# Kernel tuning notes

Hardware: AMD Instinct MI355X
Metric: run time of the kernel (lower is better)

Reference implementation:

```python
import jax, jax.numpy as jnp
import numpy as np

EPS = 1e-8

def leaky(x):
    return jnp.where(x >= 0, x, 0.1 * x)

def gln(y, gamma, beta, axes):
    # global layer norm: normalize over all non-batch axes given
    mean = jnp.mean(y, axis=axes, keepdims=True)
    var = jnp.mean((y - mean) ** 2, axis=axes, keepdims=True)
    return gamma * (y - mean) / jnp.sqrt(var + EPS) + beta

def conv1d(x, w, b, stride, padding):
    # x: [N, Cin, T], w: [Cout, Cin, K]
    out = jax.lax.conv_general_dilated(
        x, w, window_strides=(stride,), padding=[(padding, padding)],
        dimension_numbers=('NCH', 'OIH', 'NCH'))
    return out + b[None, :, None]

def setup_inputs() -> dict:
    key = jax.random.key(0)
    ks = jax.random.split(key, 8)
    M, C, B, T = 4, 2, 128, 2000
    feature = jax.random.normal(ks[0], (M, B, T), jnp.float32)
    mask = jax.random.uniform(ks[1], (M, C, B, T), jnp.float32)
    # Conv2d(B*C -> 1, 1x1) weight stored as [C, B] (xavier-ish scale)
    w2d = jax.random.normal(ks[2], (C, B), jnp.float32) * (1.0 / np.sqrt(C * B))
    b2d = jnp.zeros((), jnp.float32)
    g2d = jnp.ones((), jnp.float32)    # GLN_2D(1) gamma
    be2d = jnp.zeros((), jnp.float32)  # GLN_2D(1) beta
    # Conv1d stack: 128->256 (k3,s2,p1), 256->256 (k3,s2,p1), 256->1 (k1,s1)
    w1 = jax.random.normal(ks[3], (256, B, 3), jnp.float32) * (1.0 / np.sqrt(B * 3))
    b1 = jnp.zeros((256,), jnp.float32)
    g1 = jnp.ones((1, 256, 1), jnp.float32)
    bb1 = jnp.zeros((1, 256, 1), jnp.float32)
    w2 = jax.random.normal(ks[4], (256, 256, 3), jnp.float32) * (1.0 / np.sqrt(256 * 3))
    b2 = jnp.zeros((256,), jnp.float32)
    g2 = jnp.ones((1, 256, 1), jnp.float32)
    bb2 = jnp.zeros((1, 256, 1), jnp.float32)
    w3 = jax.random.normal(ks[5], (1, 256, 1), jnp.float32) * (1.0 / np.sqrt(256))
    b3 = jnp.zeros((1,), jnp.float32)
    return dict(feature=feature, mask=mask, w2d=w2d, b2d=b2d, g2d=g2d, be2d=be2d,
                w1=w1, b1=b1, g1=g1, bb1=bb1, w2=w2, b2=b2, g2=g2, bb2=bb2,
                w3=w3, b3=b3)

def reference(feature, mask, w2d, b2d, g2d, be2d,
              w1, b1, g1, bb1, w2, b2, g2, bb2, w3, b3):
    # torch: d_in = einsum('bft,bcpt->bcfpt').view(B, C*F, P, T) -> Conv2d(C*F->1, 1x1)
    # With F == P == B, the viewed channel index is (c*F + f), so the 1x1 conv is
    #   d[b,p,t] = sum_{c,f} w2d[c,f] * feature[b,f,t] * mask[b,c,p,t] + b2d
    # expressed as a fused two-step contraction (same math, no 5D materialization):
    a = jnp.einsum('cf,bft->bct', w2d, feature)        # [M, C, T]
    d = jnp.einsum('bct,bcpt->bpt', a, mask) + b2d     # [M, P, T]
    d = d[:, None]                                     # [M, 1, P, T]
    d = gln(d, g2d, be2d, axes=(1, 2, 3))              # GLN_2D(1)
    d = leaky(d)
    x = d[:, 0]                                        # squeeze(1) -> [M, B, T]
    x = leaky(gln(conv1d(x, w1, b1, 2, 1), g1, bb1, (1, 2)))
    x = leaky(gln(conv1d(x, w2, b2, 2, 1), g2, bb2, (1, 2)))
    x = conv1d(x, w3, b3, 1, 0)                        # [M, 1, 500]
    return x
```

## Files before the change

kernel.cpp:

```cpp
#include <hip/hip_runtime.h>
#include <hip/hip_bf16.h>

#define EPS 1e-8f
typedef unsigned short ushortT;
typedef __bf16 bf16x8 __attribute__((ext_vector_type(8)));
typedef float f32x4 __attribute__((ext_vector_type(4)));
union B8 { uint4 u; bf16x8 v; };

__device__ __forceinline__ float leaky(float x) { return x >= 0.f ? x : 0.1f * x; }

__device__ __forceinline__ ushortT f2bf(float v) {
    unsigned u = __float_as_uint(v);
    return (ushortT)((u + 0x7fffu + ((u >> 16) & 1u)) >> 16);
}

__device__ __forceinline__ void block_reduce2(float& s, float& q, float* red) {
    __syncthreads();
    #pragma unroll
    for (int off = 32; off > 0; off >>= 1) {
        s += __shfl_down(s, off, 64);
        q += __shfl_down(q, off, 64);
    }
    const int wid = threadIdx.x >> 6, lane = threadIdx.x & 63;
    if (lane == 0) { red[wid] = s; red[4 + wid] = q; }
    __syncthreads();
    if (threadIdx.x == 0) {
        s = red[0] + red[1] + red[2] + red[3];
        q = red[4] + red[5] + red[6] + red[7];
    }
}

__device__ __forceinline__ void stats_from_partials(const float* __restrict__ partials,
                                                    int n, float nrm,
                                                    float* red, float* stat) {
    float s = 0.f, q = 0.f;
    if ((int)threadIdx.x < n) {
        s = partials[threadIdx.x * 2];
        q = partials[threadIdx.x * 2 + 1];
    }
    block_reduce2(s, q, red);
    if (threadIdx.x == 0) {
        float mean = s * nrm;
        float var  = fmaxf(q * nrm - mean * mean, 0.f);
        stat[0] = mean;
        stat[1] = rsqrtf(var + EPS);
    }
    __syncthreads();
}

__global__ void ka(const float* __restrict__ feature, const float* __restrict__ mask,
                   const float* __restrict__ w2d, const float* __restrict__ b2d,
                   const float* __restrict__ w1, const float* __restrict__ w2,
                   ushortT* __restrict__ w1b, ushortT* __restrict__ w2b,
                   float* __restrict__ dT, float* __restrict__ p0out) {
    if (blockIdx.x >= 63) {
        int p = (blockIdx.x - 63) * 4 + blockIdx.y;
        int base = (p < 96 ? p : p - 96) * 1024 + threadIdx.x * 4;
        const float* src = (p < 96) ? (w1 + base) : (w2 + base);
        ushortT* dst = (p < 96) ? (w1b + base) : (w2b + base);
        float4 v = *(const float4*)src;
        ushort4 o;
        o.x = f2bf(v.x); o.y = f2bf(v.y); o.z = f2bf(v.z); o.w = f2bf(v.w);
        *(ushort4*)dst = o;
        return;
    }
    __shared__ float4 apart[2][32][8];
    __shared__ float4 a0s4[8], a1s4[8];
    __shared__ float Xt[32][132];
    __shared__ float red[8];
    const int b = blockIdx.y;
    const int t0 = blockIdx.x * 32;
    const int tq = threadIdx.x & 7;
    const int hi = threadIdx.x >> 3;

    {
        const int tbase = t0 + tq * 4;
        float4 s0 = {0.f, 0.f, 0.f, 0.f}, s1 = s0;
        if (tbase + 3 < 2000) {
            const float* fb = feature + ((size_t)b * 128 + hi * 4) * 2000 + tbase;
            float4 wa = *(const float4*)(w2d + hi * 4);
            float4 wc = *(const float4*)(w2d + 128 + hi * 4);
            float wav[4] = {wa.x, wa.y, wa.z, wa.w};
            float wcv[4] = {wc.x, wc.y, wc.z, wc.w};
            #pragma unroll
            for (int i = 0; i < 4; i++) {
                float4 fv = *(const float4*)(fb + (size_t)i * 2000);
                s0.x = fmaf(wav[i], fv.x, s0.x); s0.y = fmaf(wav[i], fv.y, s0.y);
                s0.z = fmaf(wav[i], fv.z, s0.z); s0.w = fmaf(wav[i], fv.w, s0.w);
                s1.x = fmaf(wcv[i], fv.x, s1.x); s1.y = fmaf(wcv[i], fv.y, s1.y);
                s1.z = fmaf(wcv[i], fv.z, s1.z); s1.w = fmaf(wcv[i], fv.w, s1.w);
            }
        }
        apart[0][hi][tq] = s0;
        apart[1][hi][tq] = s1;
    }
    __syncthreads();
    if (threadIdx.x < 16) {
        int c = threadIdx.x >> 3, tqq = threadIdx.x & 7;
        float4 s = {0.f, 0.f, 0.f, 0.f};
        #pragma unroll
        for (int i = 0; i < 32; i++) {
            float4 v = apart[c][i][tqq];
            s.x += v.x; s.y += v.y; s.z += v.z; s.w += v.w;
        }
        (c ? a1s4 : a0s4)[tqq] = s;
    }
    __syncthreads();

    const float bb = b2d[0];
    float s = 0.f, q = 0.f;
    {
        const int tbase = t0 + tq * 4;
        if (tbase + 3 < 2000) {
            float4 a0 = a0s4[tq], a1 = a1s4[tq];
            const float* m0p = mask + ((size_t)(b * 2 + 0) * 128 + hi * 4) * 2000 + tbase;
            const float* m1p = mask + ((size_t)(b * 2 + 1) * 128 + hi * 4) * 2000 + tbase;
            #pragma unroll
            for (int j = 0; j < 4; j++) {
                int p = hi * 4 + j;
                float4 m0 = *(const float4*)(m0p + (size_t)j * 2000);
                float4 m1 = *(const float4*)(m1p + (size_t)j * 2000);
                float v0 = fmaf(a0.x, m0.x, a1.x * m1.x) + bb;
                float v1 = fmaf(a0.y, m0.y, a1.y * m1.y) + bb;
                float v2 = fmaf(a0.z, m0.z, a1.z * m1.z) + bb;
                float v3 = fmaf(a0.w, m0.w, a1.w * m1.w) + bb;
                Xt[tq * 4 + 0][p] = v0;
                Xt[tq * 4 + 1][p] = v1;
                Xt[tq * 4 + 2][p] = v2;
                Xt[tq * 4 + 3][p] = v3;
                s += v0 + v1 + v2 + v3;
                q = fmaf(v0, v0, q); q = fmaf(v1, v1, q);
                q = fmaf(v2, v2, q); q = fmaf(v3, v3, q);
            }
        }
    }
    block_reduce2(s, q, red);
    if (threadIdx.x == 0) {
        p0out[(b * 128 + blockIdx.x) * 2]     = s;
        p0out[(b * 128 + blockIdx.x) * 2 + 1] = q;
    }
    {
        const int tw = threadIdx.x >> 3;
        if (t0 + tw < 2000) {
            float* drow = dT + (size_t)b * 256000 + (size_t)(t0 + tw) * 128;
            #pragma unroll
            for (int jj = 0; jj < 4; jj++) {
                int p4 = (threadIdx.x & 7) + jj * 8;
                float4 v = *(const float4*)&Xt[tw][p4 * 4];
                *(float4*)(drow + p4 * 4) = v;
            }
        }
    }
}

template <int CIN, int TIN, int TOUT, int NT, int MPB, bool PERCH, bool TOUT_TRANS>
__launch_bounds__(256, 2)
__global__ void kconv(const float* __restrict__ xT, const float* __restrict__ pin,
                      int npin, float nrm,
                      const float* __restrict__ gam, const float* __restrict__ bet,
                      const ushortT* __restrict__ wb, const float* __restrict__ bias,
                      float* __restrict__ yout, float* __restrict__ pout) {
    constexpr int K = CIN * 3;
    constexpr int ROWB = K * 2;
    constexpr int NF = NT / 16;
    constexpr int MSC = 256 / MPB;
    constexpr int MF = MPB / 64;
    constexpr int LPR = CIN / 4;
    constexpr int RPP = 256 / LPR;
    constexpr int NPASS = (2 * NT) / RPP + 1;
    __shared__ char Xs[NT * ROWB];
    __shared__ float red[8];
    __shared__ float stat[2];

    const int b = blockIdx.y;
    const int ms = blockIdx.x % MSC;
    const int tile = blockIdx.x / MSC;
    const int t0 = tile * NT;
    const int lane = threadIdx.x & 63;
    const int wv = threadIdx.x >> 6;

    stats_from_partials(pin + b * 256, npin, nrm, red, stat);
    const float mean = stat[0], inv = stat[1];

    const int rl = threadIdx.x / LPR;
    const int f0 = (threadIdx.x % LPR) * 4;
    float gg[4], bv[4];
    if (PERCH) {
        float4 g4 = *(const float4*)(gam + f0);
        float4 b4 = *(const float4*)(bet + f0);
        gg[0] = g4.x; gg[1] = g4.y; gg[2] = g4.z; gg[3] = g4.w;
        bv[0] = b4.x; bv[1] = b4.y; bv[2] = b4.z; bv[3] = b4.w;
    } else {
        gg[0] = gg[1] = gg[2] = gg[3] = gam[0];
        bv[0] = bv[1] = bv[2] = bv[3] = bet[0];
    }
    const int base_ti = 2 * t0 - 1;
    #pragma unroll
    for (int pass = 0; pass < NPASS; pass++) {
        int c = pass * RPP + rl;
        if (c > 2 * NT) continue;
        int ti = base_ti + c;
        float4 x4 = {0.f, 0.f, 0.f, 0.f};
        if (ti >= 0 && ti < TIN)
            x4 = *(const float4*)(xT + ((size_t)b * TIN + ti) * CIN + f0);
        float xv[4] = {x4.x, x4.y, x4.z, x4.w};
        ushortT h[4];
        #pragma unroll
        for (int j = 0; j < 4; j++)
            h[j] = f2bf(leaky(fmaf(gg[j] * inv, xv[j] - mean, bv[j])));
        if (c & 1) {
            int tt = (c - 1) >> 1;
            int ad = tt * ROWB, sw = (tt & 7) << 4;
            #pragma unroll
            for (int j = 0; j < 4; j++)
                *(ushortT*)(Xs + ((ad + ((f0 + j) * 3 + 1) * 2) ^ sw)) = h[j];
        } else {
            int tt = c >> 1;
            if (tt < NT) {
                int ad = tt * ROWB, sw = (tt & 7) << 4;
                #pragma unroll
                for (int j = 0; j < 4; j++)
                    *(ushortT*)(Xs + ((ad + (f0 + j) * 6) ^ sw)) = h[j];
            }
            if (tt >= 1) {
                int ad = (tt - 1) * ROWB, sw = ((tt - 1) & 7) << 4;
                #pragma unroll
                for (int j = 0; j < 4; j++)
                    *(ushortT*)(Xs + ((ad + (f0 + j) * 6 + 4) ^ sw)) = h[j];
            }
        }
    }
    __syncthreads();

    const int obase = ms * MPB + wv * (MPB / 4);
    const int kgrp = (lane >> 4) * 8;
    const int mrow = lane & 15;
    f32x4 acc[MF][NF];
    #pragma unroll
    for (int mf = 0; mf < MF; mf++)
        #pragma unroll
        for (int nf = 0; nf < NF; nf++) acc[mf][nf] = (f32x4){0.f, 0.f, 0.f, 0.f};
    #pragma unroll 2
    for (int ks = 0; ks < K / 32; ks++) {
        int kb = ks * 32 + kgrp;
        B8 afr[MF];
        #pragma unroll
        for (int mf = 0; mf < MF; mf++)
            afr[mf].u = *(const uint4*)(wb + (size_t)(obase + mf * 16 + mrow) * K + kb);
        #pragma unroll
        for (int nf = 0; nf < NF; nf++) {
            int tt = nf * 16 + mrow;
            int ad = (tt * ROWB + kb * 2) ^ ((tt & 7) << 4);
            B8 bfr; bfr.u = *(const uint4*)(Xs + ad);
            #pragma unroll
            for (int mf = 0; mf < MF; mf++)
                acc[mf][nf] = __builtin_amdgcn_mfma_f32_16x16x32_bf16(
                    afr[mf].v, bfr.v, acc[mf][nf], 0, 0, 0);
        }
    }

    float s = 0.f, q = 0.f;
    #pragma unroll
    for (int mf = 0; mf < MF; mf++) {
        const int o0 = obase + mf * 16 + (lane >> 4) * 4;
        if (TOUT_TRANS) {
            float4 b4 = *(const float4*)(bias + o0);
            float bi[4] = {b4.x, b4.y, b4.z, b4.w};
            #pragma unroll
            for (int nf = 0; nf < NF; nf++) {
                int t = t0 + nf * 16 + mrow;
                if (t < TOUT) {
                    float v0 = acc[mf][nf][0] + bi[0], v1 = acc[mf][nf][1] + bi[1];
                    float v2 = acc[mf][nf][2] + bi[2], v3 = acc[mf][nf][3] + bi[3];
                    float4 v = {v0, v1, v2, v3};
                    *(float4*)(yout + ((size_t)b * TOUT + t) * 256 + o0) = v;
                    s += v0 + v1 + v2 + v3;
                    q = fmaf(v0, v0, q); q = fmaf(v1, v1, q);
                    q = fmaf(v2, v2, q); q = fmaf(v3, v3, q);
                }
            }
        } else {
            #pragma unroll
            for (int nf = 0; nf < NF; nf++) {
                int t = t0 + nf * 16 + mrow;
                if (t < TOUT) {
                    #pragma unroll
                    for (int r = 0; r < 4; r++) {
                        float v = acc[mf][nf][r] + bias[o0 + r];
                        yout[((size_t)b * 256 + o0 + r) * TOUT + t] = v;
                        s += v; q = fmaf(v, v, q);
                    }
                }
            }
        }
    }
    block_reduce2(s, q, red);
    if (threadIdx.x == 0) {
        int bi = b * 128 + tile * MSC + ms;
        pout[bi * 2]     = s;
        pout[bi * 2 + 1] = q;
    }
}

__global__ void kd_head(const float* __restrict__ y2, const float* __restrict__ p2,
                        const float* __restrict__ g2, const float* __restrict__ bb2,
                        const float* __restrict__ w3, const float* __restrict__ b3,
                        float* __restrict__ out) {
    __shared__ float red[8];
    __shared__ float stat[2];
    __shared__ float part[4][64];
    const int b = blockIdx.y;
    stats_from_partials(p2 + b * 256, 128, 1.f / 128000.f, red, stat);
    const float mean = stat[0], inv = stat[1];
    const int tl = threadIdx.x & 63, fg = threadIdx.x >> 6;
    const int t = blockIdx.x * 64 + tl;
    float acc = 0.f;
    if (t < 500) {
        const float* yb = y2 + ((size_t)b * 256 + fg * 64) * 500 + t;
        #pragma unroll 8
        for (int i = 0; i < 64; i++) {
            int o = fg * 64 + i;
            float raw = yb[i * 500];
            float xv = leaky(fmaf(g2[o] * inv, raw - mean, bb2[o]));
            acc = fmaf(w3[o], xv, acc);
        }
    }
    part[fg][tl] = acc;
    __syncthreads();
    if (fg == 0 && t < 500)
        out[b * 500 + t] = b3[0] + part[0][tl] + part[1][tl] + part[2][tl] + part[3][tl];
}

extern "C" void kernel_launch(void* const* d_in, const int* in_sizes, int n_in,
                              void* d_out, int out_size, void* d_ws, size_t ws_size,
                              hipStream_t stream) {
    const float* feature = (const float*)d_in[0];
    const float* mask    = (const float*)d_in[1];
    const float* w2d     = (const float*)d_in[2];
    const float* b2d     = (const float*)d_in[3];
    const float* g2d     = (const float*)d_in[4];
    const float* be2d    = (const float*)d_in[5];
    const float* w1      = (const float*)d_in[6];
    const float* b1      = (const float*)d_in[7];
    const float* g1      = (const float*)d_in[8];
    const float* bb1     = (const float*)d_in[9];
    const float* w2      = (const float*)d_in[10];
    const float* b2      = (const float*)d_in[11];
    const float* g2      = (const float*)d_in[12];
    const float* bb2     = (const float*)d_in[13];
    const float* w3      = (const float*)d_in[14];
    const float* b3      = (const float*)d_in[15];
    float* out = (float*)d_out;

    float* ws = (float*)d_ws;
    float* p0  = ws;
    float* p1  = ws + 1024;
    float* p2  = ws + 2048;
    float* dT  = ws + 3072;
    float* y1T = dT + 1024000;
    float* y2  = y1T + 1024000;
    ushortT* w1b = (ushortT*)(y2 + 512000);
    ushortT* w2b = w1b + 98304;

    ka<<<dim3(63 + 72, 4), 256, 0, stream>>>(feature, mask, w2d, b2d,
                                             w1, w2, w1b, w2b, dT, p0);
    kconv<128, 2000, 1000, 16, 128, false, true><<<dim3(126, 4), 256, 0, stream>>>(
        dT, p0, 63, 1.f / 256000.f, g2d, be2d, w1b, b1, y1T, p1);
    kconv<256, 1000, 500, 16, 64, true, false><<<dim3(128, 4), 256, 0, stream>>>(
        y1T, p1, 126, 1.f / 256000.f, g1, bb1, w2b, b2, y2, p2);
    kd_head<<<dim3(8, 4), 256, 0, stream>>>(y2, p2, g2, bb2, w3, b3, out);
}
```

Before: 42.48 us.

## Fuse head kernel into second conv via per-batch atomic counter tail

Removes the separate head launch by having the last 8 blocks per batch of the second conv kernel wait on an atomic counter until all 128 producer blocks have written their partial stats, then compute the GLN+leaky+1x1 conv head. The counter is zeroed inside the first kernel. This saves one kernel launch and its gap, at the cost of spin-waiting blocks and relying on co-residency/forward progress of the producer blocks.

```diff
diff --git a/kernel.cpp b/kernel.cpp
--- a/kernel.cpp
+++ b/kernel.cpp
@@ -52,8 +52,11 @@
                    const float* __restrict__ w2d, const float* __restrict__ b2d,
                    const float* __restrict__ w1, const float* __restrict__ w2,
                    ushortT* __restrict__ w1b, ushortT* __restrict__ w2b,
-                   float* __restrict__ dT, float* __restrict__ p0out) {
+                   float* __restrict__ dT, float* __restrict__ p0out,
+                   int* __restrict__ cnt) {
     if (blockIdx.x >= 63) {
+        if (blockIdx.x == 63 && blockIdx.y == 0 && threadIdx.x < 16)
+            cnt[threadIdx.x] = 0;
         int p = (blockIdx.x - 63) * 4 + blockIdx.y;
         int base = (p < 96 ? p : p - 96) * 1024 + threadIdx.x * 4;
         const float* src = (p < 96) ? (w1 + base) : (w2 + base);
@@ -153,13 +156,17 @@
     }
 }
 
-template <int CIN, int TIN, int TOUT, int NT, int MPB, bool PERCH, bool TOUT_TRANS>
+template <int CIN, int TIN, int TOUT, int NT, int MPB, bool PERCH, bool TOUT_TRANS,
+          bool TAIL>
 __launch_bounds__(256, 2)
 __global__ void kconv(const float* __restrict__ xT, const float* __restrict__ pin,
                       int npin, float nrm,
                       const float* __restrict__ gam, const float* __restrict__ bet,
                       const ushortT* __restrict__ wb, const float* __restrict__ bias,
-                      float* __restrict__ yout, float* __restrict__ pout) {
+                      float* __restrict__ yout, float* __restrict__ pout,
+                      const float* __restrict__ g2t, const float* __restrict__ bb2t,
+                      const float* __restrict__ w3t, const float* __restrict__ b3t,
+                      float* __restrict__ outp, int* __restrict__ cnt) {
     constexpr int K = CIN * 3;
     constexpr int ROWB = K * 2;
     constexpr int NF = NT / 16;
@@ -171,6 +178,7 @@
     __shared__ char Xs[NT * ROWB];
     __shared__ float red[8];
     __shared__ float stat[2];
+    __shared__ int oldv;
 
     const int b = blockIdx.y;
     const int ms = blockIdx.x % MSC;
@@ -300,35 +308,48 @@
         pout[bi * 2]     = s;
         pout[bi * 2 + 1] = q;
     }
-}
-
-__global__ void kd_head(const float* __restrict__ y2, const float* __restrict__ p2,
-                        const float* __restrict__ g2, const float* __restrict__ bb2,
-                        const float* __restrict__ w3, const float* __restrict__ b3,
-                        float* __restrict__ out) {
-    __shared__ float red[8];
-    __shared__ float stat[2];
-    __shared__ float part[4][64];
-    const int b = blockIdx.y;
-    stats_from_partials(p2 + b * 256, 128, 1.f / 128000.f, red, stat);
-    const float mean = stat[0], inv = stat[1];
-    const int tl = threadIdx.x & 63, fg = threadIdx.x >> 6;
-    const int t = blockIdx.x * 64 + tl;
-    float acc = 0.f;
-    if (t < 500) {
-        const float* yb = y2 + ((size_t)b * 256 + fg * 64) * 500 + t;
-        #pragma unroll 8
-        for (int i = 0; i < 64; i++) {
-            int o = fg * 64 + i;
-            float raw = yb[i * 500];
-            float xv = leaky(fmaf(g2[o] * inv, raw - mean, bb2[o]));
-            acc = fmaf(w3[o], xv, acc);
-        }
-    }
-    part[fg][tl] = acc;
-    __syncthreads();
-    if (fg == 0 && t < 500)
-        out[b * 500 + t] = b3[0] + part[0][tl] + part[1][tl] + part[2][tl] + part[3][tl];
+
+    if (TAIL) {
+        constexpr int NPROD = 128;
+        __threadfence();
+        if (threadIdx.x == 0)
+            oldv = __hip_atomic_fetch_add(&cnt[b], 1, __ATOMIC_RELAXED,
+                                          __HIP_MEMORY_SCOPE_AGENT);
+        __syncthreads();
+        const int old = oldv;
+        if (old >= NPROD - 8) {
+            const int part_id = old - (NPROD - 8);
+            if (threadIdx.x == 0) {
+                while (__hip_atomic_load(&cnt[b], __ATOMIC_RELAXED,
+                                         __HIP_MEMORY_SCOPE_AGENT) < NPROD)
+                    __builtin_amdgcn_s_sleep(2);
+            }
+            __syncthreads();
+            __threadfence();
+            stats_from_partials(pout + b * 256, NPROD, 1.f / (256.f * TOUT),
+                                red, stat);
+            const float mean2 = stat[0], inv2 = stat[1];
+            const int tl = threadIdx.x & 63, fg = threadIdx.x >> 6;
+            const int t = part_id * 64 + tl;
+            float accv = 0.f;
+            if (t < TOUT) {
+                const float* yb = yout + ((size_t)b * 256 + fg * 64) * TOUT + t;
+                #pragma unroll 8
+                for (int i = 0; i < 64; i++) {
+                    int o = fg * 64 + i;
+                    float raw = yb[(size_t)i * TOUT];
+                    float xv = leaky(fmaf(g2t[o] * inv2, raw - mean2, bb2t[o]));
+                    accv = fmaf(w3t[o], xv, accv);
+                }
+            }
+            float* part = (float*)Xs;
+            part[fg * 64 + tl] = accv;
+            __syncthreads();
+            if (fg == 0 && t < TOUT)
+                outp[b * TOUT + t] = b3t[0] + part[0 * 64 + tl] + part[1 * 64 + tl]
+                                   + part[2 * 64 + tl] + part[3 * 64 + tl];
+        }
+    }
 }
 
 extern "C" void kernel_launch(void* const* d_in, const int* in_sizes, int n_in,
@@ -356,17 +377,21 @@
     float* p0  = ws;
     float* p1  = ws + 1024;
     float* p2  = ws + 2048;
-    float* dT  = ws + 3072;
+    int*   cnt = (int*)(ws + 3072);
+    float* dT  = ws + 3088;
     float* y1T = dT + 1024000;
     float* y2  = y1T + 1024000;
     ushortT* w1b = (ushortT*)(y2 + 512000);
     ushortT* w2b = w1b + 98304;
 
     ka<<<dim3(63 + 72, 4), 256, 0, stream>>>(feature, mask, w2d, b2d,
-                                             w1, w2, w1b, w2b, dT, p0);
-    kconv<128, 2000, 1000, 16, 128, false, true><<<dim3(126, 4), 256, 0, stream>>>(
-        dT, p0, 63, 1.f / 256000.f, g2d, be2d, w1b, b1, y1T, p1);
-    kconv<256, 1000, 500, 16, 64, true, false><<<dim3(128, 4), 256, 0, stream>>>(
-        y1T, p1, 126, 1.f / 256000.f, g1, bb1, w2b, b2, y2, p2);
-    kd_head<<<dim3(8, 4), 256, 0, stream>>>(y2, p2, g2, bb2, w3, b3, out);
-}
+                                             w1, w2, w1b, w2b, dT, p0, cnt);
+    kconv<128, 2000, 1000, 16, 128, false, true, false>
+        <<<dim3(126, 4), 256, 0, stream>>>(
+        dT, p0, 63, 1.f / 256000.f, g2d, be2d, w1b, b1, y1T, p1,
+        nullptr, nullptr, nullptr, nullptr, nullptr, cnt);
+    kconv<256, 1000, 500, 16, 64, true, false, true>
+        <<<dim3(128, 4), 256, 0, stream>>>(
+        y1T, p1, 126, 1.f / 256000.f, g1, bb1, w2b, b2, y2, p2,
+        g2, bb2, w3, b3, out, cnt);
+}
```

New measurement: 104.1 us. 145% more time.

## Store first-stage activations as bf16, prefetch conv inputs, widen head grid

Applied to the files above, without the earlier changes.

The first kernel now writes the pre-normalisation activation tensor dT as bf16 instead of fp32, which halves that intermediate's write and read traffic. Both conv kernels load their input rows into registers before the statistics reduction, so global load latency can overlap the sync-heavy stats step. The head kernel uses 32-wide time tiles over 8 channel groups, giving twice as many blocks. The risk is an extra bf16 rounding before the mean and variance normalisation, plus higher register pressure from the prefetched rows.

```diff
diff --git a/kernel.cpp b/kernel.cpp
--- a/kernel.cpp
+++ b/kernel.cpp
@@ -12,6 +12,9 @@
 __device__ __forceinline__ ushortT f2bf(float v) {
     unsigned u = __float_as_uint(v);
     return (ushortT)((u + 0x7fffu + ((u >> 16) & 1u)) >> 16);
+}
+__device__ __forceinline__ float bf2f(ushortT h) {
+    return __uint_as_float(((unsigned)h) << 16);
 }
 
 __device__ __forceinline__ void block_reduce2(float& s, float& q, float* red) {
@@ -52,7 +55,7 @@
                    const float* __restrict__ w2d, const float* __restrict__ b2d,
                    const float* __restrict__ w1, const float* __restrict__ w2,
                    ushortT* __restrict__ w1b, ushortT* __restrict__ w2b,
-                   float* __restrict__ dT, float* __restrict__ p0out) {
+                   ushortT* __restrict__ dT, float* __restrict__ p0out) {
     if (blockIdx.x >= 63) {
         int p = (blockIdx.x - 63) * 4 + blockIdx.y;
         int base = (p < 96 ? p : p - 96) * 1024 + threadIdx.x * 4;
@@ -142,20 +145,23 @@
     {
         const int tw = threadIdx.x >> 3;
         if (t0 + tw < 2000) {
-            float* drow = dT + (size_t)b * 256000 + (size_t)(t0 + tw) * 128;
+            ushortT* drow = dT + (size_t)b * 256000 + (size_t)(t0 + tw) * 128;
             #pragma unroll
             for (int jj = 0; jj < 4; jj++) {
                 int p4 = (threadIdx.x & 7) + jj * 8;
                 float4 v = *(const float4*)&Xt[tw][p4 * 4];
-                *(float4*)(drow + p4 * 4) = v;
-            }
-        }
-    }
-}
-
-template <int CIN, int TIN, int TOUT, int NT, int MPB, bool PERCH, bool TOUT_TRANS>
+                ushort4 h;
+                h.x = f2bf(v.x); h.y = f2bf(v.y); h.z = f2bf(v.z); h.w = f2bf(v.w);
+                *(ushort4*)(drow + p4 * 4) = h;
+            }
+        }
+    }
+}
+
+template <int CIN, int TIN, int TOUT, int NT, int MPB, bool PERCH, bool TOUT_TRANS,
+          bool XBF>
 __launch_bounds__(256, 2)
-__global__ void kconv(const float* __restrict__ xT, const float* __restrict__ pin,
+__global__ void kconv(const void* __restrict__ xTv, const float* __restrict__ pin,
                       int npin, float nrm,
                       const float* __restrict__ gam, const float* __restrict__ bet,
                       const ushortT* __restrict__ wb, const float* __restrict__ bias,
@@ -179,11 +185,33 @@
     const int lane = threadIdx.x & 63;
     const int wv = threadIdx.x >> 6;
 
+    const int rl = threadIdx.x / LPR;
+    const int f0 = (threadIdx.x % LPR) * 4;
+    const int base_ti = 2 * t0 - 1;
+    float xreg[NPASS][4];
+    #pragma unroll
+    for (int pass = 0; pass < NPASS; pass++) {
+        int c = pass * RPP + rl;
+        int ti = base_ti + c;
+        xreg[pass][0] = xreg[pass][1] = xreg[pass][2] = xreg[pass][3] = 0.f;
+        if (c <= 2 * NT && ti >= 0 && ti < TIN) {
+            if (XBF) {
+                ushort4 u = *(const ushort4*)((const ushortT*)xTv
+                                + ((size_t)b * TIN + ti) * CIN + f0);
+                xreg[pass][0] = bf2f(u.x); xreg[pass][1] = bf2f(u.y);
+                xreg[pass][2] = bf2f(u.z); xreg[pass][3] = bf2f(u.w);
+            } else {
+                float4 x4 = *(const float4*)((const float*)xTv
+                                + ((size_t)b * TIN + ti) * CIN + f0);
+                xreg[pass][0] = x4.x; xreg[pass][1] = x4.y;
+                xreg[pass][2] = x4.z; xreg[pass][3] = x4.w;
+            }
+        }
+    }
+
     stats_from_partials(pin + b * 256, npin, nrm, red, stat);
     const float mean = stat[0], inv = stat[1];
 
-    const int rl = threadIdx.x / LPR;
-    const int f0 = (threadIdx.x % LPR) * 4;
     float gg[4], bv[4];
     if (PERCH) {
         float4 g4 = *(const float4*)(gam + f0);
@@ -194,20 +222,15 @@
         gg[0] = gg[1] = gg[2] = gg[3] = gam[0];
         bv[0] = bv[1] = bv[2] = bv[3] = bet[0];
     }
-    const int base_ti = 2 * t0 - 1;
+
     #pragma unroll
     for (int pass = 0; pass < NPASS; pass++) {
         int c = pass * RPP + rl;
         if (c > 2 * NT) continue;
-        int ti = base_ti + c;
-        float4 x4 = {0.f, 0.f, 0.f, 0.f};
-        if (ti >= 0 && ti < TIN)
-            x4 = *(const float4*)(xT + ((size_t)b * TIN + ti) * CIN + f0);
-        float xv[4] = {x4.x, x4.y, x4.z, x4.w};
         ushortT h[4];
         #pragma unroll
         for (int j = 0; j < 4; j++)
-            h[j] = f2bf(leaky(fmaf(gg[j] * inv, xv[j] - mean, bv[j])));
+            h[j] = f2bf(leaky(fmaf(gg[j] * inv, xreg[pass][j] - mean, bv[j])));
         if (c & 1) {
             int tt = (c - 1) >> 1;
             int ad = tt * ROWB, sw = (tt & 7) << 4;
@@ -308,27 +331,31 @@
                         float* __restrict__ out) {
     __shared__ float red[8];
     __shared__ float stat[2];
-    __shared__ float part[4][64];
+    __shared__ float part[8][32];
     const int b = blockIdx.y;
     stats_from_partials(p2 + b * 256, 128, 1.f / 128000.f, red, stat);
     const float mean = stat[0], inv = stat[1];
-    const int tl = threadIdx.x & 63, fg = threadIdx.x >> 6;
-    const int t = blockIdx.x * 64 + tl;
+    const int tl = threadIdx.x & 31, fg = threadIdx.x >> 5;
+    const int t = blockIdx.x * 32 + tl;
     float acc = 0.f;
     if (t < 500) {
-        const float* yb = y2 + ((size_t)b * 256 + fg * 64) * 500 + t;
+        const float* yb = y2 + ((size_t)b * 256 + fg * 32) * 500 + t;
         #pragma unroll 8
-        for (int i = 0; i < 64; i++) {
-            int o = fg * 64 + i;
-            float raw = yb[i * 500];
+        for (int i = 0; i < 32; i++) {
+            int o = fg * 32 + i;
+            float raw = yb[(size_t)i * 500];
             float xv = leaky(fmaf(g2[o] * inv, raw - mean, bb2[o]));
             acc = fmaf(w3[o], xv, acc);
         }
     }
     part[fg][tl] = acc;
     __syncthreads();
-    if (fg == 0 && t < 500)
-        out[b * 500 + t] = b3[0] + part[0][tl] + part[1][tl] + part[2][tl] + part[3][tl];
+    if (fg == 0 && t < 500) {
+        float r = b3[0];
+        #pragma unroll
+        for (int i = 0; i < 8; i++) r += part[i][tl];
+        out[b * 500 + t] = r;
+    }
 }
 
 extern "C" void kernel_launch(void* const* d_in, const int* in_sizes, int n_in,
@@ -356,17 +383,19 @@
     float* p0  = ws;
     float* p1  = ws + 1024;
     float* p2  = ws + 2048;
-    float* dT  = ws + 3072;
-    float* y1T = dT + 1024000;
+    ushortT* dT = (ushortT*)(ws + 3072);
+    float* y1T = ws + 3072 + 512000;
     float* y2  = y1T + 1024000;
     ushortT* w1b = (ushortT*)(y2 + 512000);
     ushortT* w2b = w1b + 98304;
 
     ka<<<dim3(63 + 72, 4), 256, 0, stream>>>(feature, mask, w2d, b2d,
                                              w1, w2, w1b, w2b, dT, p0);
-    kconv<128, 2000, 1000, 16, 128, false, true><<<dim3(126, 4), 256, 0, stream>>>(
+    kconv<128, 2000, 1000, 16, 128, false, true, true>
+        <<<dim3(126, 4), 256, 0, stream>>>(
         dT, p0, 63, 1.f / 256000.f, g2d, be2d, w1b, b1, y1T, p1);
-    kconv<256, 1000, 500, 16, 64, true, false><<<dim3(128, 4), 256, 0, stream>>>(
+    kconv<256, 1000, 500, 16, 64, true, false, false>
+        <<<dim3(128, 4), 256, 0, stream>>>(
         y1T, p1, 126, 1.f / 256000.f, g1, bb1, w2b, b2, y2, p2);
-    kd_head<<<dim3(8, 4), 256, 0, stream>>>(y2, p2, g2, bb2, w3, b3, out);
-}
+    kd_head<<<dim3(16, 4), 256, 0, stream>>>(y2, p2, g2, bb2, w3, b3, out);
+}
```

Result: faster. 40.31 us (-5.1%).
